# Performance work log

Hardware: AMD Instinct MI355X
Metric: run time of the kernel (lower is better)

The kernel has to match this reference:

```python
import jax, jax.numpy as jnp
import numpy as np

N, E, D_IN, H, OUT = 50000, 800000, 128, 256, 2
BN_EPS = 1e-5
LN_EPS = 1e-5


def _xavier(k, fi, fo):
    lim = float(np.sqrt(6.0 / (fi + fo)))
    return jax.random.uniform(k, (fi, fo), minval=-lim, maxval=lim, dtype=jnp.float32)


def setup_inputs() -> dict:
    key = jax.random.key(0)
    ks = jax.random.split(key, 8)
    return {
        "x": jax.random.normal(ks[0], (N, D_IN), dtype=jnp.float32),
        "edge_index": jax.random.randint(ks[1], (2, E), 0, N, dtype=jnp.int32),
        "feature_scale": jnp.ones((D_IN,), jnp.float32),
        "feature_bias": jnp.zeros((D_IN,), jnp.float32),
        "bn0_g": jnp.ones((D_IN,), jnp.float32),
        "bn0_b": jnp.zeros((D_IN,), jnp.float32),
        "W1": _xavier(ks[2], D_IN, H), "b1": jnp.zeros((H,), jnp.float32),
        "bn1_g": jnp.ones((H,), jnp.float32), "bn1_b": jnp.zeros((H,), jnp.float32),
        "ln1_g": jnp.ones((H,), jnp.float32), "ln1_b": jnp.zeros((H,), jnp.float32),
        "W2": _xavier(ks[3], H, H), "b2": jnp.zeros((H,), jnp.float32),
        "bn2_g": jnp.ones((H,), jnp.float32), "bn2_b": jnp.zeros((H,), jnp.float32),
        "ln2_g": jnp.ones((H,), jnp.float32), "ln2_b": jnp.zeros((H,), jnp.float32),
        "Wout": _xavier(ks[4], H, OUT), "bout": jnp.zeros((OUT,), jnp.float32),
    }


def _batchnorm(x, g, b):
    # training-mode BatchNorm1d: batch stats over node axis, biased variance
    mu = jnp.mean(x, axis=0)
    var = jnp.mean(jnp.square(x - mu), axis=0)
    return g * (x - mu) * jax.lax.rsqrt(var + BN_EPS) + b


def _layernorm(x, g, b):
    mu = jnp.mean(x, axis=-1, keepdims=True)
    var = jnp.mean(jnp.square(x - mu), axis=-1, keepdims=True)
    return g * (x - mu) * jax.lax.rsqrt(var + LN_EPS) + b


def _gcn(x, W, b, src, dst, dinv):
    # PyG GCNConv with self-loops: D^{-1/2}(A+I)D^{-1/2} X W + b
    h = x @ W                                   # [N, F]
    norm = (dinv[src] * dinv[dst])[:, None]     # [E, 1]
    msg = h[src] * norm                         # [E, F] (dominant traffic)
    agg = jax.ops.segment_sum(msg, dst, num_segments=N)
    return agg + (dinv * dinv)[:, None] * h + b


def _forward(x, feature_scale, feature_bias, bn0_g, bn0_b,
             W1, b1, bn1_g, bn1_b, ln1_g, ln1_b,
             W2, b2, bn2_g, bn2_b, ln2_g, ln2_b,
             Wout, bout, edge_index):
    src, dst = edge_index[0], edge_index[1]
    deg = jax.ops.segment_sum(jnp.ones((E,), x.dtype), dst, num_segments=N) + 1.0
    dinv = jax.lax.rsqrt(deg)

    h = x * feature_scale + feature_bias
    h = _batchnorm(h, bn0_g, bn0_b)            # input_bn; dropout = identity (eval)

    # layer 0 (no residual: i == 0)
    h1 = _gcn(h, W1, b1, src, dst, dinv)
    h1 = jax.nn.relu(h1)
    h1 = _batchnorm(h1, bn1_g, bn1_b)
    h1 = _layernorm(h1, ln1_g, ln1_b)

    # layer 1 (residual add, shapes match)
    h2 = _gcn(h1, W2, b2, src, dst, dinv)
    h2 = jax.nn.relu(h2)
    h2 = _batchnorm(h2, bn2_g, bn2_b)
    h2 = _layernorm(h2, ln2_g, ln2_b)
    h2 = h2 + h1

    return h2 @ Wout + bout


def reference(x, edge_index, feature_scale, feature_bias, bn0_g, bn0_b,
              W1, b1, bn1_g, bn1_b, ln1_g, ln1_b,
              W2, b2, bn2_g, bn2_b, ln2_g, ln2_b,
              Wout, bout):
    return _forward(x, feature_scale, feature_bias, bn0_g, bn0_b,
                    W1, b1, bn1_g, bn1_b, ln1_g, ln1_b,
                    W2, b2, bn2_g, bn2_b, ln2_g, ln2_b,
                    Wout, bout, edge_index)
```

## Files before the change

### kernel.cpp

```cpp
#include <hip/hip_runtime.h>
#include <hip/hip_bf16.h>
#include <stdint.h>

#define N_NODES 50000
#define N_EDGES 800000
#define D_IN    128
#define H_DIM   256
#define BN_EPS  1e-5f
#define LN_EPS  1e-5f
#define NBLK2 782
#define SLICE_ELEMS ((size_t)N_NODES * 32)
#define BN0_BLOCKS 1024
#define PREPX_BLOCKS 6250
#define TR_BLOCKS 256
#define NBKT 196
#define CHUNK 2048
#define RCHUNKS 391

typedef float v4f __attribute__((ext_vector_type(4)));
typedef float v2f __attribute__((ext_vector_type(2)));
typedef short v8s __attribute__((ext_vector_type(8)));
typedef unsigned v4u __attribute__((ext_vector_type(4)));

__device__ __forceinline__ float bflo(unsigned u){ return __uint_as_float(u << 16); }
__device__ __forceinline__ float bfhi(unsigned u){ return __uint_as_float(u & 0xffff0000u); }
__device__ __forceinline__ unsigned short f2bf(float f){
  unsigned u = __float_as_uint(f);
  u += 0x7fffu + ((u >> 16) & 1u);
  return (unsigned short)(u >> 16);
}
__device__ __forceinline__ unsigned pack2(float a, float b){
  return (unsigned)f2bf(a) | ((unsigned)f2bf(b) << 16);
}

__device__ __forceinline__ int block_excl_scan(int v){
  int t = threadIdx.x;
  int lane = t & 63, w = t >> 6;
  int inc = v;
  #pragma unroll
  for (int m = 1; m < 64; m <<= 1){
    int o = __shfl_up(inc, m, 64);
    if (lane >= m) inc += o;
  }
  __shared__ int wsum[4];
  if (lane == 63) wsum[w] = inc;
  __syncthreads();
  int base = 0;
  #pragma unroll
  for (int j = 0; j < 4; ++j) if (j < w) base += wsum[j];
  return base + inc - v;
}

__global__ __launch_bounds__(256) void bn0r1_k(const int* ei, const float* x,
                                               const float* fs, const float* fb,
                                               float* S, float* Q, int* ghist){
  int b = blockIdx.x, t = threadIdx.x;
  if (b >= BN0_BLOCKS){
    __shared__ int lh[NBKT];
    int b2 = b - BN0_BLOCKS;
    for (int i = t; i < NBKT; i += 256) lh[i] = 0;
    __syncthreads();
    int e0 = b2 * CHUNK;
    int n = min(CHUNK, N_EDGES - e0);
    for (int i = t; i < n; i += 256)
      atomicAdd(&lh[ei[N_EDGES + e0 + i] >> 8], 1);
    __syncthreads();
    if (t < NBKT && lh[t] > 0) atomicAdd(&ghist[t], lh[t]);
    return;
  }
  int cl = t & 31, rg = t >> 5;
  int c = cl * 4;
  float4 fs4 = *(const float4*)(fs + c);
  float4 fb4 = *(const float4*)(fb + c);
  float s0=0,s1=0,s2=0,s3=0,q0=0,q1=0,q2=0,q3=0;
  for (int row = b * 8 + rg; row < N_NODES; row += BN0_BLOCKS * 8){
    float4 xv = *(const float4*)(x + (size_t)row * D_IN + c);
    float v0 = xv.x * fs4.x + fb4.x;
    float v1 = xv.y * fs4.y + fb4.y;
    float v2 = xv.z * fs4.z + fb4.z;
    float v3 = xv.w * fs4.w + fb4.w;
    s0 += v0; s1 += v1; s2 += v2; s3 += v3;
    q0 += v0*v0; q1 += v1*v1; q2 += v2*v2; q3 += v3*v3;
  }
  __shared__ float red[256][8];
  red[t][0]=s0; red[t][1]=s1; red[t][2]=s2; red[t][3]=s3;
  red[t][4]=q0; red[t][5]=q1; red[t][6]=q2; red[t][7]=q3;
  __syncthreads();
  float* Sr = S + (b & 7) * D_IN;
  float* Qr = Q + (b & 7) * D_IN;
  if (t < 32){
    float a[8];
    #pragma unroll
    for (int i = 0; i < 8; ++i) a[i] = red[t][i];
    for (int j = 1; j < 8; ++j)
      #pragma unroll
      for (int i = 0; i < 8; ++i) a[i] += red[t + 32*j][i];
    #pragma unroll
    for (int i = 0; i < 4; ++i){ atomicAdd(&Sr[t*4+i], a[i]); atomicAdd(&Qr[t*4+i], a[4+i]); }
  }
}

__global__ __launch_bounds__(256) void r3_k(const int* ei, const int* ghist, int* gcursor, unsigned* ebuf){
  __shared__ unsigned short dstS[CHUNK];
  __shared__ int lh[NBKT], cb[NBKT], sbb[NBKT];
  int t = threadIdx.x;
  int v = (t < NBKT) ? ghist[t] : 0;
  int epre = block_excl_scan(v);
  if (t < NBKT){ sbb[t] = epre; lh[t] = 0; }
  __syncthreads();
  int e0 = blockIdx.x * CHUNK;
  int n = min(CHUNK, N_EDGES - e0);
  for (int i = t; i < n; i += 256){
    int d = ei[N_EDGES + e0 + i];
    dstS[i] = (unsigned short)d;
    atomicAdd(&lh[d >> 8], 1);
  }
  __syncthreads();
  if (t < NBKT && lh[t] > 0) cb[t] = sbb[t] + atomicAdd(&gcursor[t], lh[t]);
  __syncthreads();
  if (t < NBKT) lh[t] = 0;
  __syncthreads();
  for (int i = t; i < n; i += 256){
    int d = dstS[i];
    int bkt = d >> 8;
    int r = atomicAdd(&lh[bkt], 1);
    unsigned src = (unsigned)ei[e0 + i];
    ebuf[cb[bkt] + r] = ((unsigned)(d & 255) << 16) | src;
  }
}

__global__ __launch_bounds__(256) void sortprep_k(const unsigned* ebuf, const int* ghist,
                                                  int* perm, int* offs, float* dinv,
                                                  unsigned short* edges,
                                                  const float* x, const float* S, const float* Q,
                                                  const float* fs, const float* fb,
                                                  const float* gg, const float* bb,
                                                  unsigned short* xt,
                                                  const float* W1, const float* W2,
                                                  unsigned short* W1t, unsigned short* W2t){
  int b = blockIdx.x, t = threadIdx.x;
  if (b < NBKT){
    __shared__ int h[256], dh[128], ep_s[128], W_s[128], lc[128], curs[256], sbb[NBKT + 1];
    int gv = (t < NBKT) ? ghist[t] : 0;
    int gpre = block_excl_scan(gv);
    if (t < NBKT) sbb[t] = gpre;
    if (t == NBKT - 1) sbb[NBKT] = gpre + gv;
    h[t] = 0;
    if (t < 128){ dh[t] = 0; lc[t] = 0; }
    __syncthreads();
    int lo = sbb[b], hi = sbb[b + 1];
    for (int i = lo + t; i < hi; i += 256)
      atomicAdd(&h[(ebuf[i] >> 16) & 255], 1);
    __syncthreads();
    int node = b * 256 + t;
    bool valid = node < N_NODES;
    int deg = valid ? h[t] : 0;
    if (valid) atomicAdd(&dh[min(deg, 127)], 1);
    __syncthreads();
    int cv = (t < 128) ? dh[t] : 0;
    int e1 = block_excl_scan(cv);
    __syncthreads();
    int e2 = block_excl_scan((t < 128) ? cv * t : 0);
    __syncthreads();
    if (t < 128){ ep_s[t] = e1; W_s[t] = e2; }
    __syncthreads();
    if (valid){
      int bin = min(deg, 127);
      int r = atomicAdd(&lc[bin], 1);
      int pl = ep_s[bin] + r;
      int pos = b * 256 + pl;
      int off = lo + W_s[bin] + (pl - ep_s[bin]) * deg;
      perm[pos] = node;
      offs[pos] = off;
      dinv[node] = rsqrtf((float)deg + 1.0f);
      curs[t] = off;
    }
    __syncthreads();
    for (int i = lo + t; i < hi; i += 256){
      unsigned u = ebuf[i];
      int l8 = (u >> 16) & 255;
      int pos = atomicAdd(&curs[l8], 1);
      edges[pos] = (unsigned short)(u & 0xffffu);
    }
    if (b == 0 && t == 0) offs[N_NODES] = N_EDGES;
    return;
  }
  if (b < NBKT + PREPX_BLOCKS){
    int i = (b - NBKT) * 256 + t;
    int row = i >> 5; int c = (i & 31) * 4;
    float4 Sv = *(const float4*)(S + c);
    float4 Qv = *(const float4*)(Q + c);
    #pragma unroll
    for (int rep = 1; rep < 8; ++rep){
      float4 s2 = *(const float4*)(S + rep * D_IN + c);
      float4 q2 = *(const float4*)(Q + rep * D_IN + c);
      Sv.x += s2.x; Sv.y += s2.y; Sv.z += s2.z; Sv.w += s2.w;
      Qv.x += q2.x; Qv.y += q2.y; Qv.z += q2.z; Qv.w += q2.w;
    }
    float4 fs4 = *(const float4*)(fs + c);
    float4 fb4 = *(const float4*)(fb + c);
    float4 gg4 = *(const float4*)(gg + c);
    float4 bb4 = *(const float4*)(bb + c);
    const float invN = 1.0f / N_NODES;
    float mu0 = Sv.x*invN, mu1 = Sv.y*invN, mu2 = Sv.z*invN, mu3 = Sv.w*invN;
    float r0 = rsqrtf(Qv.x*invN - mu0*mu0 + BN_EPS);
    float r1 = rsqrtf(Qv.y*invN - mu1*mu1 + BN_EPS);
    float r2 = rsqrtf(Qv.z*invN - mu2*mu2 + BN_EPS);
    float r3 = rsqrtf(Qv.w*invN - mu3*mu3 + BN_EPS);
    float a0 = gg4.x*r0*fs4.x, c0 = gg4.x*r0*(fb4.x - mu0) + bb4.x;
    float a1 = gg4.y*r1*fs4.y, c1 = gg4.y*r1*(fb4.y - mu1) + bb4.y;
    float a2 = gg4.z*r2*fs4.z, c2 = gg4.z*r2*(fb4.z - mu2) + bb4.z;
    float a3 = gg4.w*r3*fs4.w, c3 = gg4.w*r3*(fb4.w - mu3) + bb4.w;
    float4 xv = *(const float4*)(x + (size_t)row * D_IN + c);
    uint2 o;
    o.x = pack2(a0 * xv.x + c0, a1 * xv.y + c1);
    o.y = pack2(a2 * xv.z + c2, a3 * xv.w + c3);
    *(uint2*)(xt + (size_t)row * D_IN + c) = o;
    return;
  }
  int i = (b - NBKT - PREPX_BLOCKS) * 256 + t;
  if (i < D_IN * H_DIM){
    int r = i / H_DIM, c = i % H_DIM;
    W1t[c * D_IN + r] = f2bf(W1[i]);
  }
  if (i < H_DIM * H_DIM){
    int r = i / H_DIM, c = i % H_DIM;
    W2t[c * H_DIM + r] = f2bf(W2[i]);
  }
}

template<int K>
__global__ __launch_bounds__(256) void gemm_k(const unsigned short* A, const unsigned short* Bt,
                                              const float* dinv, unsigned short* C, int M){
  __shared__ __align__(16) short smem[16896];
  __shared__ float dvs[64];
  short* As = smem;
  short* Bs = smem + 64 * 40;
  int t = threadIdx.x;
  int m0 = blockIdx.x * 64;
  int lane = t & 63;
  int w = t >> 6;
  int fr = lane & 15, quad = lane >> 4;
  if (t < 64) dvs[t] = (m0 + t < M) ? dinv[m0 + t] : 0.0f;
  v4f acc[4][4] = {};
  int sr = t >> 2;
  int sk = (t & 3) << 3;
  for (int k0 = 0; k0 < K; k0 += 32){
    __syncthreads();
    uint4 av = {0,0,0,0};
    int arow = m0 + sr;
    if (arow < M) av = *(const uint4*)(A + (size_t)arow * K + k0 + sk);
    *(uint4*)(&As[sr * 40 + sk]) = av;
    #pragma unroll
    for (int j = 0; j < 4; ++j){
      int brow = sr + 64 * j;
      uint4 bv = *(const uint4*)(Bt + (size_t)brow * K + k0 + sk);
      *(uint4*)(&Bs[brow * 40 + sk]) = bv;
    }
    __syncthreads();
    v8s af[4], bf[4];
    #pragma unroll
    for (int mi = 0; mi < 4; ++mi)
      af[mi] = *(const v8s*)(&As[(mi * 16 + fr) * 40 + quad * 8]);
    #pragma unroll
    for (int ni = 0; ni < 4; ++ni)
      bf[ni] = *(const v8s*)(&Bs[(w * 64 + ni * 16 + fr) * 40 + quad * 8]);
    #pragma unroll
    for (int mi = 0; mi < 4; ++mi)
      #pragma unroll
      for (int ni = 0; ni < 4; ++ni)
        acc[mi][ni] = __builtin_amdgcn_mfma_f32_16x16x32_bf16(af[mi], bf[ni], acc[mi][ni], 0, 0, 0);
  }
  __syncthreads();
  short* Cs = smem;
  #pragma unroll
  for (int mi = 0; mi < 4; ++mi)
    #pragma unroll
    for (int ni = 0; ni < 4; ++ni)
      #pragma unroll
      for (int r = 0; r < 4; ++r){
        int row = mi * 16 + quad * 4 + r;
        int col = w * 64 + ni * 16 + fr;
        Cs[row * 264 + col] = (short)f2bf(acc[mi][ni][r] * dvs[row]);
      }
  __syncthreads();
  int orow = t >> 2;
  int grow = m0 + orow;
  if (grow < M){
    #pragma unroll
    for (int j = 0; j < 4; ++j){
      int oc = (t & 3) * 16 + 64 * j;
      v8s v0 = *(const v8s*)(&Cs[orow * 264 + oc]);
      v8s v1 = *(const v8s*)(&Cs[orow * 264 + oc + 8]);
      *(v8s*)(&C[(size_t)(oc >> 5) * SLICE_ELEMS + (size_t)grow * 32 + (oc & 31)]) = v0;
      int oc1 = oc + 8;
      *(v8s*)(&C[(size_t)(oc1 >> 5) * SLICE_ELEMS + (size_t)grow * 32 + (oc1 & 31)]) = v1;
    }
  }
}

#define ACCP(u, A) { v2f d_ = {bflo(u), bfhi(u)}; A += d_; }
#define ACC8(vv) ACCP(vv.x, A0) ACCP(vv.y, A1) ACCP(vv.z, A2) ACCP(vv.w, A3)

__global__ __launch_bounds__(256, 4) void agg_k(const unsigned short* hs, const int* offsets,
                                                const unsigned short* edges, const int* perm,
                                                const float* dinv, const float* bias,
                                                unsigned short* g, float* pS, float* pQ){
  __shared__ float wps[4][4][16];
  int t = threadIdx.x;
  int lane = t & 63;
  int wv = t >> 6;
  int slice = blockIdx.x & 7;
  int l4 = lane & 3;
  int grp = blockIdx.x >> 3;
  int nb = grp * 64;
  int idx = nb + (t >> 2);
  bool act = idx < N_NODES;
  int node = act ? perm[idx] : 0;
  float dvv = act ? dinv[node] : 0.f;
  const uint4* hb4 = (const uint4*)(hs + (size_t)slice * SLICE_ELEMS);
  const unsigned* ew = (const unsigned*)edges;
  float4 bb0 = *(const float4*)(bias + slice * 32 + l4 * 8);
  float4 bb1 = *(const float4*)(bias + slice * 32 + l4 * 8 + 4);
  uint4 sv = hb4[(size_t)node * 4 + l4];
  v2f A0 = {bflo(sv.x), bfhi(sv.x)};
  v2f A1 = {bflo(sv.y), bfhi(sv.y)};
  v2f A2 = {bflo(sv.z), bfhi(sv.z)};
  v2f A3 = {bflo(sv.w), bfhi(sv.w)};
  int e  = act ? offsets[idx] : 0;
  int e1 = act ? offsets[idx + 1] : 0;
  if ((e & 1) && e < e1){
    unsigned d = ew[e >> 1];
    uint4 vv = hb4[(size_t)(d >> 16) * 4 + l4];
    ACC8(vv);
    ++e;
  }
  for (; e + 16 <= e1; e += 16){
    int ru = e >> 1;
    unsigned dd[8];
    #pragma unroll
    for (int j = 0; j < 8; ++j) dd[j] = ew[ru + j];
    uint4 v[16];
    #pragma unroll
    for (int j = 0; j < 8; ++j){
      v[2*j]   = hb4[(size_t)(dd[j] & 0xffffu) * 4 + l4];
      v[2*j+1] = hb4[(size_t)(dd[j] >> 16)     * 4 + l4];
    }
    #pragma unroll
    for (int j = 0; j < 16; ++j){ ACC8(v[j]); }
  }
  if (e + 8 <= e1){
    int ru = e >> 1;
    unsigned dd[4];
    #pragma unroll
    for (int j = 0; j < 4; ++j) dd[j] = ew[ru + j];
    uint4 v[8];
    #pragma unroll
    for (int j = 0; j < 4; ++j){
      v[2*j]   = hb4[(size_t)(dd[j] & 0xffffu) * 4 + l4];
      v[2*j+1] = hb4[(size_t)(dd[j] >> 16)     * 4 + l4];
    }
    #pragma unroll
    for (int j = 0; j < 8; ++j){ ACC8(v[j]); }
    e += 8;
  }
  if (e + 4 <= e1){
    int ru = e >> 1;
    unsigned dd0 = ew[ru], dd1 = ew[ru + 1];
    uint4 v[4];
    v[0] = hb4[(size_t)(dd0 & 0xffffu) * 4 + l4];
    v[1] = hb4[(size_t)(dd0 >> 16)     * 4 + l4];
    v[2] = hb4[(size_t)(dd1 & 0xffffu) * 4 + l4];
    v[3] = hb4[(size_t)(dd1 >> 16)     * 4 + l4];
    #pragma unroll
    for (int j = 0; j < 4; ++j){ ACC8(v[j]); }
    e += 4;
  }
  for (; e < e1; ++e){
    unsigned d = ew[e >> 1];
    unsigned s = (e & 1) ? (d >> 16) : (d & 0xffffu);
    uint4 vv = hb4[(size_t)s * 4 + l4];
    ACC8(vv);
  }
  float y0 = act ? fmaxf(dvv * A0.x + bb0.x, 0.f) : 0.f;
  float y1 = act ? fmaxf(dvv * A0.y + bb0.y, 0.f) : 0.f;
  float y2 = act ? fmaxf(dvv * A1.x + bb0.z, 0.f) : 0.f;
  float y3 = act ? fmaxf(dvv * A1.y + bb0.w, 0.f) : 0.f;
  float y4 = act ? fmaxf(dvv * A2.x + bb1.x, 0.f) : 0.f;
  float y5 = act ? fmaxf(dvv * A2.y + bb1.y, 0.f) : 0.f;
  float y6 = act ? fmaxf(dvv * A3.x + bb1.z, 0.f) : 0.f;
  float y7 = act ? fmaxf(dvv * A3.y + bb1.w, 0.f) : 0.f;
  if (act){
    v4u o;
    o.x = pack2(y0, y1); o.y = pack2(y2, y3);
    o.z = pack2(y4, y5); o.w = pack2(y6, y7);
    __builtin_nontemporal_store(o, (v4u*)(g + (size_t)node * H_DIM + slice * 32 + l4 * 8));
  }
  float q0 = y0*y0, q1 = y1*y1, q2 = y2*y2, q3 = y3*y3;
  float q4 = y4*y4, q5 = y5*y5, q6 = y6*y6, q7 = y7*y7;
  #pragma unroll
  for (int m = 4; m < 64; m <<= 1){
    y0 += __shfl_xor(y0, m, 64); y1 += __shfl_xor(y1, m, 64);
    y2 += __shfl_xor(y2, m, 64); y3 += __shfl_xor(y3, m, 64);
    y4 += __shfl_xor(y4, m, 64); y5 += __shfl_xor(y5, m, 64);
    y6 += __shfl_xor(y6, m, 64); y7 += __shfl_xor(y7, m, 64);
    q0 += __shfl_xor(q0, m, 64); q1 += __shfl_xor(q1, m, 64);
    q2 += __shfl_xor(q2, m, 64); q3 += __shfl_xor(q3, m, 64);
    q4 += __shfl_xor(q4, m, 64); q5 += __shfl_xor(q5, m, 64);
    q6 += __shfl_xor(q6, m, 64); q7 += __shfl_xor(q7, m, 64);
  }
  if (lane < 4){
    wps[wv][lane][0] = y0; wps[wv][lane][1] = y1; wps[wv][lane][2] = y2; wps[wv][lane][3] = y3;
    wps[wv][lane][4] = y4; wps[wv][lane][5] = y5; wps[wv][lane][6] = y6; wps[wv][lane][7] = y7;
    wps[wv][lane][8] = q0; wps[wv][lane][9] = q1; wps[wv][lane][10] = q2; wps[wv][lane][11] = q3;
    wps[wv][lane][12] = q4; wps[wv][lane][13] = q5; wps[wv][lane][14] = q6; wps[wv][lane][15] = q7;
  }
  __syncthreads();
  if (t < 64){
    int tl = t >> 4, ti = t & 15;
    float v = wps[0][tl][ti] + wps[1][tl][ti] + wps[2][tl][ti] + wps[3][tl][ti];
    int col32 = tl * 8 + (ti & 7);
    if (ti < 8) pS[(size_t)blockIdx.x * 32 + col32] = v;
    else        pQ[(size_t)blockIdx.x * 32 + col32] = v;
  }
}

__global__ __launch_bounds__(1024) void redu_k(const float* pS, const float* pQ,
                                               const float* gg, const float* bb,
                                               float* sc, float* sh){
  __shared__ float ls[32][32], lq[32][32];
  int t = threadIdx.x;
  int slice = blockIdx.x;
  int grp = t >> 5, c32 = t & 31;
  float as = 0.f, aq = 0.f;
  for (int blk2 = grp; blk2 < NBLK2; blk2 += 32){
    size_t o = ((size_t)blk2 * 8 + slice) * 32 + c32;
    as += pS[o]; aq += pQ[o];
  }
  ls[grp][c32] = as; lq[grp][c32] = aq;
  __syncthreads();
  if (t < 32){
    float S = 0.f, Q = 0.f;
    #pragma unroll
    for (int gI = 0; gI < 32; ++gI){ S += ls[gI][t]; Q += lq[gI][t]; }
    int col = slice * 32 + t;
    const float invN = 1.0f / N_NODES;
    float mu = S * invN;
    float rs = rsqrtf(Q * invN - mu * mu + BN_EPS);
    float s = gg[col] * rs;
    sc[col] = s;
    sh[col] = bb[col] - s * mu;
  }
}

__global__ __launch_bounds__(256) void apply1_k(const unsigned short* g, const float* sc, const float* sh,
                                                const float* lng, const float* lnb, unsigned short* h1){
  int t = threadIdx.x;
  int lane32 = t & 31;
  int row = blockIdx.x * 8 + (t >> 5);
  if (row >= N_NODES) return;
  int c = lane32 * 8;
  float4 s40 = *(const float4*)(sc + c);
  float4 s41 = *(const float4*)(sc + c + 4);
  float4 h40 = *(const float4*)(sh + c);
  float4 h41 = *(const float4*)(sh + c + 4);
  uint4 u = *(const uint4*)(g + (size_t)row * H_DIM + c);
  float v0 = s40.x * bflo(u.x) + h40.x;
  float v1 = s40.y * bfhi(u.x) + h40.y;
  float v2 = s40.z * bflo(u.y) + h40.z;
  float v3 = s40.w * bfhi(u.y) + h40.w;
  float v4 = s41.x * bflo(u.z) + h41.x;
  float v5 = s41.y * bfhi(u.z) + h41.y;
  float v6 = s41.z * bflo(u.w) + h41.z;
  float v7 = s41.w * bfhi(u.w) + h41.w;
  float sum = v0+v1+v2+v3+v4+v5+v6+v7;
  float sq  = v0*v0+v1*v1+v2*v2+v3*v3+v4*v4+v5*v5+v6*v6+v7*v7;
  #pragma unroll
  for (int m = 1; m < 32; m <<= 1){ sum += __shfl_xor(sum, m, 64); sq += __shfl_xor(sq, m, 64); }
  float mu = sum * (1.0f / H_DIM);
  float var = sq * (1.0f / H_DIM) - mu * mu;
  float rs = rsqrtf(var + LN_EPS);
  float4 g40 = *(const float4*)(lng + c);
  float4 g41 = *(const float4*)(lng + c + 4);
  float4 b40 = *(const float4*)(lnb + c);
  float4 b41 = *(const float4*)(lnb + c + 4);
  uint4 o;
  o.x = pack2(g40.x * (v0 - mu) * rs + b40.x, g40.y * (v1 - mu) * rs + b40.y);
  o.y = pack2(g40.z * (v2 - mu) * rs + b40.z, g40.w * (v3 - mu) * rs + b40.w);
  o.z = pack2(g41.x * (v4 - mu) * rs + b41.x, g41.y * (v5 - mu) * rs + b41.y);
  o.w = pack2(g41.z * (v6 - mu) * rs + b41.z, g41.w * (v7 - mu) * rs + b41.w);
  *(uint4*)(h1 + (size_t)row * H_DIM + c) = o;
}

__global__ __launch_bounds__(256) void apply2_k(const unsigned short* g, const float* sc, const float* sh,
                                                const float* lng, const float* lnb,
                                                const unsigned short* h1, const float* Wout,
                                                const float* bout, float* out){
  int t = threadIdx.x;
  int lane32 = t & 31;
  int row = blockIdx.x * 8 + (t >> 5);
  if (row >= N_NODES) return;
  int c = lane32 * 8;
  float4 s40 = *(const float4*)(sc + c);
  float4 s41 = *(const float4*)(sc + c + 4);
  float4 h40 = *(const float4*)(sh + c);
  float4 h41 = *(const float4*)(sh + c + 4);
  uint4 u = *(const uint4*)(g + (size_t)row * H_DIM + c);
  float v0 = s40.x * bflo(u.x) + h40.x;
  float v1 = s40.y * bfhi(u.x) + h40.y;
  float v2 = s40.z * bflo(u.y) + h40.z;
  float v3 = s40.w * bfhi(u.y) + h40.w;
  float v4 = s41.x * bflo(u.z) + h41.x;
  float v5 = s41.y * bfhi(u.z) + h41.y;
  float v6 = s41.z * bflo(u.w) + h41.z;
  float v7 = s41.w * bfhi(u.w) + h41.w;
  float sum = v0+v1+v2+v3+v4+v5+v6+v7;
  float sq  = v0*v0+v1*v1+v2*v2+v3*v3+v4*v4+v5*v5+v6*v6+v7*v7;
  #pragma unroll
  for (int m = 1; m < 32; m <<= 1){ sum += __shfl_xor(sum, m, 64); sq += __shfl_xor(sq, m, 64); }
  float mu = sum * (1.0f / H_DIM);
  float var = sq * (1.0f / H_DIM) - mu * mu;
  float rs = rsqrtf(var + LN_EPS);
  float4 g40 = *(const float4*)(lng + c);
  float4 g41 = *(const float4*)(lng + c + 4);
  float4 b40 = *(const float4*)(lnb + c);
  float4 b41 = *(const float4*)(lnb + c + 4);
  uint4 hr = *(const uint4*)(h1 + (size_t)row * H_DIM + c);
  float y0 = g40.x * (v0 - mu) * rs + b40.x + bflo(hr.x);
  float y1 = g40.y * (v1 - mu) * rs + b40.y + bfhi(hr.x);
  float y2 = g40.z * (v2 - mu) * rs + b40.z + bflo(hr.y);
  float y3 = g40.w * (v3 - mu) * rs + b40.w + bfhi(hr.y);
  float y4 = g41.x * (v4 - mu) * rs + b41.x + bflo(hr.z);
  float y5 = g41.y * (v5 - mu) * rs + b41.y + bfhi(hr.z);
  float y6 = g41.z * (v6 - mu) * rs + b41.z + bflo(hr.w);
  float y7 = g41.w * (v7 - mu) * rs + b41.w + bfhi(hr.w);
  float4 w0 = *(const float4*)(Wout + c * 2);
  float4 w1 = *(const float4*)(Wout + c * 2 + 4);
  float4 w2 = *(const float4*)(Wout + c * 2 + 8);
  float4 w3 = *(const float4*)(Wout + c * 2 + 12);
  float o0 = y0*w0.x + y1*w0.z + y2*w1.x + y3*w1.z + y4*w2.x + y5*w2.z + y6*w3.x + y7*w3.z;
  float o1 = y0*w0.y + y1*w0.w + y2*w1.y + y3*w1.w + y4*w2.y + y5*w2.w + y6*w3.y + y7*w3.w;
  #pragma unroll
  for (int m = 1; m < 32; m <<= 1){ o0 += __shfl_xor(o0, m, 64); o1 += __shfl_xor(o1, m, 64); }
  if (lane32 == 0){
    out[(size_t)row * 2 + 0] = o0 + bout[0];
    out[(size_t)row * 2 + 1] = o1 + bout[1];
  }
}

extern "C" void kernel_launch(void* const* d_in, const int* in_sizes, int n_in,
                              void* d_out, int out_size, void* d_ws, size_t ws_size,
                              hipStream_t stream) {
  const float* x    = (const float*)d_in[0];
  const int*   ei   = (const int*)d_in[1];
  const float* fs   = (const float*)d_in[2];
  const float* fb   = (const float*)d_in[3];
  const float* bn0g = (const float*)d_in[4];
  const float* bn0b = (const float*)d_in[5];
  const float* W1   = (const float*)d_in[6];
  const float* b1   = (const float*)d_in[7];
  const float* bn1g = (const float*)d_in[8];
  const float* bn1b = (const float*)d_in[9];
  const float* ln1g = (const float*)d_in[10];
  const float* ln1b = (const float*)d_in[11];
  const float* W2   = (const float*)d_in[12];
  const float* b2   = (const float*)d_in[13];
  const float* bn2g = (const float*)d_in[14];
  const float* bn2b = (const float*)d_in[15];
  const float* ln2g = (const float*)d_in[16];
  const float* ln2b = (const float*)d_in[17];
  const float* Wout = (const float*)d_in[18];
  const float* bout = (const float*)d_in[19];
  float* out = (float*)d_out;

  char* w = (char*)d_ws;
  float* bn0S  = (float*)(w + 0);
  float* bn0Q  = (float*)(w + 4096);
  int*   ghist  = (int*)(w + 8192);
  int*   gcursor= (int*)(w + 8976);
  const size_t ZERO_BYTES = 9760;
  float* sc1   = (float*)(w + 10240);
  float* sh1   = (float*)(w + 11264);
  float* sc2   = (float*)(w + 12288);
  float* sh2   = (float*)(w + 13312);
  float* dinv  = (float*)(w + 211584);
  int*   offs  = (int*)(w + 411584);
  int*   perm  = (int*)(w + 611712);
  unsigned short* edges = (unsigned short*)(w + 1011712);
  unsigned short* xt   = (unsigned short*)(w + 2611712);
  unsigned short* W1t  = (unsigned short*)(w + 15411712);
  unsigned short* W2t  = (unsigned short*)(w + 15477248);
  unsigned short* hlin = (unsigned short*)(w + 15608320);
  unsigned*       ebuf = (unsigned*)(w + 15608320);
  unsigned short* gbuf = (unsigned short*)(w + 41208320);
  unsigned short* h1   = (unsigned short*)(w + 66808320);
  float* pS    = (float*)(w + 92408320);
  float* pQ    = (float*)(w + 94008832);

  (void)in_sizes; (void)n_in; (void)out_size; (void)ws_size;

  hipMemsetAsync(d_ws, 0, ZERO_BYTES, stream);

  bn0r1_k<<<BN0_BLOCKS + RCHUNKS, 256, 0, stream>>>(ei, x, fs, fb, bn0S, bn0Q, ghist);
  r3_k<<<RCHUNKS, 256, 0, stream>>>(ei, ghist, gcursor, ebuf);
  sortprep_k<<<NBKT + PREPX_BLOCKS + TR_BLOCKS, 256, 0, stream>>>(
      ebuf, ghist, perm, offs, dinv, edges, x, bn0S, bn0Q, fs, fb, bn0g, bn0b, xt, W1, W2, W1t, W2t);

  int ggrid = (N_NODES + 63) / 64;
  int agg_blocks = NBLK2 * 8;

  gemm_k<D_IN><<<ggrid, 256, 0, stream>>>(xt, W1t, dinv, hlin, N_NODES);
  agg_k<<<agg_blocks, 256, 0, stream>>>(hlin, offs, edges, perm, dinv, b1, gbuf, pS, pQ);
  redu_k<<<8, 1024, 0, stream>>>(pS, pQ, bn1g, bn1b, sc1, sh1);
  apply1_k<<<(N_NODES + 7) / 8, 256, 0, stream>>>(gbuf, sc1, sh1, ln1g, ln1b, h1);

  gemm_k<H_DIM><<<ggrid, 256, 0, stream>>>(h1, W2t, dinv, hlin, N_NODES);
  agg_k<<<agg_blocks, 256, 0, stream>>>(hlin, offs, edges, perm, dinv, b2, gbuf, pS, pQ);
  redu_k<<<8, 1024, 0, stream>>>(pS, pQ, bn2g, bn2b, sc2, sh2);
  apply2_k<<<(N_NODES + 7) / 8, 256, 0, stream>>>(gbuf, sc2, sh2, ln2g, ln2b, h1, Wout, bout, out);
}
```

Baseline: 344.6 us.

## Stage edge lists in LDS, halve agg block size, parallelize BN stat reduction

The aggregation kernel now uses 128-thread blocks covering 32 nodes. Each block first copies its contiguous CSR edge segment into shared memory, so the per-node loops read neighbor indices from LDS instead of global memory, with a global fallback when the segment exceeds the chunk. The BN statistics reduction is spread over 64 blocks that atomically add into zeroed global sums. The scale and shift are now computed inside the apply kernels. In exchange, every block pays a barrier and a preload, more partial rows must be reduced, and float atomics make the sum order nondeterministic.

```diff
diff --git a/kernel.cpp b/kernel.cpp
--- a/kernel.cpp
+++ b/kernel.cpp
@@ -8,8 +8,10 @@
 #define H_DIM   256
 #define BN_EPS  1e-5f
 #define LN_EPS  1e-5f
-#define NBLK2 782
+#define NBLK2 1563
 #define SLICE_ELEMS ((size_t)N_NODES * 32)
+#define EDGE_CHUNK 2048
+#define AGG_T 128
 #define BN0_BLOCKS 1024
 #define PREPX_BLOCKS 6250
 #define TR_BLOCKS 256
@@ -302,24 +304,33 @@
 #define ACCP(u, A) { v2f d_ = {bflo(u), bfhi(u)}; A += d_; }
 #define ACC8(vv) ACCP(vv.x, A0) ACCP(vv.y, A1) ACCP(vv.z, A2) ACCP(vv.w, A3)
 
-__global__ __launch_bounds__(256, 4) void agg_k(const unsigned short* hs, const int* offsets,
+__global__ __launch_bounds__(128, 8) void agg_k(const unsigned short* hs, const int* offsets,
                                                 const unsigned short* edges, const int* perm,
                                                 const float* dinv, const float* bias,
                                                 unsigned short* g, float* pS, float* pQ){
-  __shared__ float wps[4][4][16];
+  __shared__ unsigned eds32[EDGE_CHUNK / 2];
+  __shared__ float wps[2][4][16];
   int t = threadIdx.x;
   int lane = t & 63;
   int wv = t >> 6;
   int slice = blockIdx.x & 7;
   int l4 = lane & 3;
   int grp = blockIdx.x >> 3;
-  int nb = grp * 64;
+  int nb = grp * 32;
   int idx = nb + (t >> 2);
+  int lastn = min(nb + 32, N_NODES);
+  int blk0 = offsets[nb];
+  int base = blk0 & ~1;
+  int blkN = offsets[lastn];
+  const unsigned* gsrc = (const unsigned*)(edges + base);
+  int nu = min((blkN - base + 1) >> 1, EDGE_CHUNK / 2);
+  for (int i = t; i < nu; i += AGG_T)
+    eds32[i] = gsrc[i];
+  __syncthreads();
   bool act = idx < N_NODES;
   int node = act ? perm[idx] : 0;
   float dvv = act ? dinv[node] : 0.f;
   const uint4* hb4 = (const uint4*)(hs + (size_t)slice * SLICE_ELEMS);
-  const unsigned* ew = (const unsigned*)edges;
   float4 bb0 = *(const float4*)(bias + slice * 32 + l4 * 8);
   float4 bb1 = *(const float4*)(bias + slice * 32 + l4 * 8 + 4);
   uint4 sv = hb4[(size_t)node * 4 + l4];
@@ -330,16 +341,22 @@
   int e  = act ? offsets[idx] : 0;
   int e1 = act ? offsets[idx + 1] : 0;
   if ((e & 1) && e < e1){
-    unsigned d = ew[e >> 1];
+    int ru = (e - base) >> 1;
+    unsigned d = (ru < EDGE_CHUNK / 2) ? eds32[ru] : gsrc[ru];
     uint4 vv = hb4[(size_t)(d >> 16) * 4 + l4];
     ACC8(vv);
     ++e;
   }
   for (; e + 16 <= e1; e += 16){
-    int ru = e >> 1;
+    int ru = (e - base) >> 1;
     unsigned dd[8];
-    #pragma unroll
-    for (int j = 0; j < 8; ++j) dd[j] = ew[ru + j];
+    if (ru + 8 <= EDGE_CHUNK / 2){
+      #pragma unroll
+      for (int j = 0; j < 8; ++j) dd[j] = eds32[ru + j];
+    } else {
+      #pragma unroll
+      for (int j = 0; j < 8; ++j) dd[j] = gsrc[ru + j];
+    }
     uint4 v[16];
     #pragma unroll
     for (int j = 0; j < 8; ++j){
@@ -350,10 +367,15 @@
     for (int j = 0; j < 16; ++j){ ACC8(v[j]); }
   }
   if (e + 8 <= e1){
-    int ru = e >> 1;
+    int ru = (e - base) >> 1;
     unsigned dd[4];
-    #pragma unroll
-    for (int j = 0; j < 4; ++j) dd[j] = ew[ru + j];
+    if (ru + 4 <= EDGE_CHUNK / 2){
+      #pragma unroll
+      for (int j = 0; j < 4; ++j) dd[j] = eds32[ru + j];
+    } else {
+      #pragma unroll
+      for (int j = 0; j < 4; ++j) dd[j] = gsrc[ru + j];
+    }
     uint4 v[8];
     #pragma unroll
     for (int j = 0; j < 4; ++j){
@@ -365,8 +387,13 @@
     e += 8;
   }
   if (e + 4 <= e1){
-    int ru = e >> 1;
-    unsigned dd0 = ew[ru], dd1 = ew[ru + 1];
+    int ru = (e - base) >> 1;
+    unsigned dd0, dd1;
+    if (ru + 2 <= EDGE_CHUNK / 2){
+      dd0 = eds32[ru]; dd1 = eds32[ru + 1];
+    } else {
+      dd0 = gsrc[ru]; dd1 = gsrc[ru + 1];
+    }
     uint4 v[4];
     v[0] = hb4[(size_t)(dd0 & 0xffffu) * 4 + l4];
     v[1] = hb4[(size_t)(dd0 >> 16)     * 4 + l4];
@@ -377,8 +404,9 @@
     e += 4;
   }
   for (; e < e1; ++e){
-    unsigned d = ew[e >> 1];
-    unsigned s = (e & 1) ? (d >> 16) : (d & 0xffffu);
+    int r = e - base;
+    unsigned d = ((r >> 1) < EDGE_CHUNK / 2) ? eds32[r >> 1] : gsrc[r >> 1];
+    unsigned s = (r & 1) ? (d >> 16) : (d & 0xffffu);
     uint4 vv = hb4[(size_t)s * 4 + l4];
     ACC8(vv);
   }
@@ -418,7 +446,7 @@
   __syncthreads();
   if (t < 64){
     int tl = t >> 4, ti = t & 15;
-    float v = wps[0][tl][ti] + wps[1][tl][ti] + wps[2][tl][ti] + wps[3][tl][ti];
+    float v = wps[0][tl][ti] + wps[1][tl][ti];
     int col32 = tl * 8 + (ti & 7);
     if (ti < 8) pS[(size_t)blockIdx.x * 32 + col32] = v;
     else        pQ[(size_t)blockIdx.x * 32 + col32] = v;
@@ -426,15 +454,15 @@
 }
 
 __global__ __launch_bounds__(1024) void redu_k(const float* pS, const float* pQ,
-                                               const float* gg, const float* bb,
-                                               float* sc, float* sh){
+                                               float* Sg, float* Qg){
   __shared__ float ls[32][32], lq[32][32];
   int t = threadIdx.x;
-  int slice = blockIdx.x;
+  int slice = blockIdx.x & 7;
+  int part = blockIdx.x >> 3;
   int grp = t >> 5, c32 = t & 31;
   float as = 0.f, aq = 0.f;
-  for (int blk2 = grp; blk2 < NBLK2; blk2 += 32){
-    size_t o = ((size_t)blk2 * 8 + slice) * 32 + c32;
+  for (int b2 = part + grp * 8; b2 < NBLK2; b2 += 256){
+    size_t o = ((size_t)b2 * 8 + slice) * 32 + c32;
     as += pS[o]; aq += pQ[o];
   }
   ls[grp][c32] = as; lq[grp][c32] = aq;
@@ -443,36 +471,46 @@
     float S = 0.f, Q = 0.f;
     #pragma unroll
     for (int gI = 0; gI < 32; ++gI){ S += ls[gI][t]; Q += lq[gI][t]; }
-    int col = slice * 32 + t;
-    const float invN = 1.0f / N_NODES;
-    float mu = S * invN;
-    float rs = rsqrtf(Q * invN - mu * mu + BN_EPS);
-    float s = gg[col] * rs;
-    sc[col] = s;
-    sh[col] = bb[col] - s * mu;
-  }
-}
-
-__global__ __launch_bounds__(256) void apply1_k(const unsigned short* g, const float* sc, const float* sh,
+    atomicAdd(&Sg[slice * 32 + t], S);
+    atomicAdd(&Qg[slice * 32 + t], Q);
+  }
+}
+
+__global__ __launch_bounds__(256) void apply1_k(const unsigned short* g,
+                                                const float* Sg, const float* Qg,
+                                                const float* bng, const float* bnb,
                                                 const float* lng, const float* lnb, unsigned short* h1){
   int t = threadIdx.x;
   int lane32 = t & 31;
   int row = blockIdx.x * 8 + (t >> 5);
   if (row >= N_NODES) return;
   int c = lane32 * 8;
-  float4 s40 = *(const float4*)(sc + c);
-  float4 s41 = *(const float4*)(sc + c + 4);
-  float4 h40 = *(const float4*)(sh + c);
-  float4 h41 = *(const float4*)(sh + c + 4);
+  const float invN = 1.0f / N_NODES;
+  float4 S0 = *(const float4*)(Sg + c), S1 = *(const float4*)(Sg + c + 4);
+  float4 Q0 = *(const float4*)(Qg + c), Q1 = *(const float4*)(Qg + c + 4);
+  float4 G0 = *(const float4*)(bng + c), G1 = *(const float4*)(bng + c + 4);
+  float4 B0 = *(const float4*)(bnb + c), B1 = *(const float4*)(bnb + c + 4);
+  float Sa[8] = {S0.x,S0.y,S0.z,S0.w,S1.x,S1.y,S1.z,S1.w};
+  float Qa[8] = {Q0.x,Q0.y,Q0.z,Q0.w,Q1.x,Q1.y,Q1.z,Q1.w};
+  float Ga[8] = {G0.x,G0.y,G0.z,G0.w,G1.x,G1.y,G1.z,G1.w};
+  float Ba[8] = {B0.x,B0.y,B0.z,B0.w,B1.x,B1.y,B1.z,B1.w};
+  float scv[8], shv[8];
+  #pragma unroll
+  for (int j = 0; j < 8; ++j){
+    float mu = Sa[j] * invN;
+    float rs = rsqrtf(Qa[j] * invN - mu * mu + BN_EPS);
+    float s = Ga[j] * rs;
+    scv[j] = s; shv[j] = Ba[j] - s * mu;
+  }
   uint4 u = *(const uint4*)(g + (size_t)row * H_DIM + c);
-  float v0 = s40.x * bflo(u.x) + h40.x;
-  float v1 = s40.y * bfhi(u.x) + h40.y;
-  float v2 = s40.z * bflo(u.y) + h40.z;
-  float v3 = s40.w * bfhi(u.y) + h40.w;
-  float v4 = s41.x * bflo(u.z) + h41.x;
-  float v5 = s41.y * bfhi(u.z) + h41.y;
-  float v6 = s41.z * bflo(u.w) + h41.z;
-  float v7 = s41.w * bfhi(u.w) + h41.w;
+  float v0 = scv[0] * bflo(u.x) + shv[0];
+  float v1 = scv[1] * bfhi(u.x) + shv[1];
+  float v2 = scv[2] * bflo(u.y) + shv[2];
+  float v3 = scv[3] * bfhi(u.y) + shv[3];
+  float v4 = scv[4] * bflo(u.z) + shv[4];
+  float v5 = scv[5] * bfhi(u.z) + shv[5];
+  float v6 = scv[6] * bflo(u.w) + shv[6];
+  float v7 = scv[7] * bfhi(u.w) + shv[7];
   float sum = v0+v1+v2+v3+v4+v5+v6+v7;
   float sq  = v0*v0+v1*v1+v2*v2+v3*v3+v4*v4+v5*v5+v6*v6+v7*v7;
   #pragma unroll
@@ -492,7 +530,9 @@
   *(uint4*)(h1 + (size_t)row * H_DIM + c) = o;
 }
 
-__global__ __launch_bounds__(256) void apply2_k(const unsigned short* g, const float* sc, const float* sh,
+__global__ __launch_bounds__(256) void apply2_k(const unsigned short* g,
+                                                const float* Sg, const float* Qg,
+                                                const float* bng, const float* bnb,
                                                 const float* lng, const float* lnb,
                                                 const unsigned short* h1, const float* Wout,
                                                 const float* bout, float* out){
@@ -501,19 +541,32 @@
   int row = blockIdx.x * 8 + (t >> 5);
   if (row >= N_NODES) return;
   int c = lane32 * 8;
-  float4 s40 = *(const float4*)(sc + c);
-  float4 s41 = *(const float4*)(sc + c + 4);
-  float4 h40 = *(const float4*)(sh + c);
-  float4 h41 = *(const float4*)(sh + c + 4);
+  const float invN = 1.0f / N_NODES;
+  float4 S0 = *(const float4*)(Sg + c), S1 = *(const float4*)(Sg + c + 4);
+  float4 Q0 = *(const float4*)(Qg + c), Q1 = *(const float4*)(Qg + c + 4);
+  float4 G0 = *(const float4*)(bng + c), G1 = *(const float4*)(bng + c + 4);
+  float4 B0 = *(const float4*)(bnb + c), B1 = *(const float4*)(bnb + c + 4);
+  float Sa[8] = {S0.x,S0.y,S0.z,S0.w,S1.x,S1.y,S1.z,S1.w};
+  float Qa[8] = {Q0.x,Q0.y,Q0.z,Q0.w,Q1.x,Q1.y,Q1.z,Q1.w};
+  float Ga[8] = {G0.x,G0.y,G0.z,G0.w,G1.x,G1.y,G1.z,G1.w};
+  float Ba[8] = {B0.x,B0.y,B0.z,B0.w,B1.x,B1.y,B1.z,B1.w};
+  float scv[8], shv[8];
+  #pragma unroll
+  for (int j = 0; j < 8; ++j){
+    float mu = Sa[j] * invN;
+    float rs = rsqrtf(Qa[j] * invN - mu * mu + BN_EPS);
+    float s = Ga[j] * rs;
+    scv[j] = s; shv[j] = Ba[j] - s * mu;
+  }
   uint4 u = *(const uint4*)(g + (size_t)row * H_DIM + c);
-  float v0 = s40.x * bflo(u.x) + h40.x;
-  float v1 = s40.y * bfhi(u.x) + h40.y;
-  float v2 = s40.z * bflo(u.y) + h40.z;
-  float v3 = s40.w * bfhi(u.y) + h40.w;
-  float v4 = s41.x * bflo(u.z) + h41.x;
-  float v5 = s41.y * bfhi(u.z) + h41.y;
-  float v6 = s41.z * bflo(u.w) + h41.z;
-  float v7 = s41.w * bfhi(u.w) + h41.w;
+  float v0 = scv[0] * bflo(u.x) + shv[0];
+  float v1 = scv[1] * bfhi(u.x) + shv[1];
+  float v2 = scv[2] * bflo(u.y) + shv[2];
+  float v3 = scv[3] * bfhi(u.y) + shv[3];
+  float v4 = scv[4] * bflo(u.z) + shv[4];
+  float v5 = scv[5] * bfhi(u.z) + shv[5];
+  float v6 = scv[6] * bflo(u.w) + shv[6];
+  float v7 = scv[7] * bfhi(u.w) + shv[7];
   float sum = v0+v1+v2+v3+v4+v5+v6+v7;
   float sq  = v0*v0+v1*v1+v2*v2+v3*v3+v4*v4+v5*v5+v6*v6+v7*v7;
   #pragma unroll
@@ -578,11 +631,11 @@
   float* bn0Q  = (float*)(w + 4096);
   int*   ghist  = (int*)(w + 8192);
   int*   gcursor= (int*)(w + 8976);
-  const size_t ZERO_BYTES = 9760;
-  float* sc1   = (float*)(w + 10240);
-  float* sh1   = (float*)(w + 11264);
-  float* sc2   = (float*)(w + 12288);
-  float* sh2   = (float*)(w + 13312);
+  float* Sg1   = (float*)(w + 9760);
+  float* Qg1   = (float*)(w + 10784);
+  float* Sg2   = (float*)(w + 11808);
+  float* Qg2   = (float*)(w + 12832);
+  const size_t ZERO_BYTES = 13856;
   float* dinv  = (float*)(w + 211584);
   int*   offs  = (int*)(w + 411584);
   int*   perm  = (int*)(w + 611712);
@@ -610,12 +663,12 @@
   int agg_blocks = NBLK2 * 8;
 
   gemm_k<D_IN><<<ggrid, 256, 0, stream>>>(xt, W1t, dinv, hlin, N_NODES);
-  agg_k<<<agg_blocks, 256, 0, stream>>>(hlin, offs, edges, perm, dinv, b1, gbuf, pS, pQ);
-  redu_k<<<8, 1024, 0, stream>>>(pS, pQ, bn1g, bn1b, sc1, sh1);
-  apply1_k<<<(N_NODES + 7) / 8, 256, 0, stream>>>(gbuf, sc1, sh1, ln1g, ln1b, h1);
+  agg_k<<<agg_blocks, AGG_T, 0, stream>>>(hlin, offs, edges, perm, dinv, b1, gbuf, pS, pQ);
+  redu_k<<<64, 1024, 0, stream>>>(pS, pQ, Sg1, Qg1);
+  apply1_k<<<(N_NODES + 7) / 8, 256, 0, stream>>>(gbuf, Sg1, Qg1, bn1g, bn1b, ln1g, ln1b, h1);
 
   gemm_k<H_DIM><<<ggrid, 256, 0, stream>>>(h1, W2t, dinv, hlin, N_NODES);
-  agg_k<<<agg_blocks, 256, 0, stream>>>(hlin, offs, edges, perm, dinv, b2, gbuf, pS, pQ);
-  redu_k<<<8, 1024, 0, stream>>>(pS, pQ, bn2g, bn2b, sc2, sh2);
-  apply2_k<<<(N_NODES + 7) / 8, 256, 0, stream>>>(gbuf, sc2, sh2, ln2g, ln2b, h1, Wout, bout, out);
-}
+  agg_k<<<agg_blocks, AGG_T, 0, stream>>>(hlin, offs, edges, perm, dinv, b2, gbuf, pS, pQ);
+  redu_k<<<64, 1024, 0, stream>>>(pS, pQ, Sg2, Qg2);
+  apply2_k<<<(N_NODES + 7) / 8, 256, 0, stream>>>(gbuf, Sg2, Qg2, bn2g, bn2b, ln2g, ln2b, h1, Wout, bout, out);
+}
```

Result: slower. 373.9 us (+8.5%).
